# Kernel optimization log

Hardware: AMD Instinct MI355X
Metric: run time of the kernel (lower is better)

Reference implementation:

```python
import jax, jax.numpy as jnp
import numpy as np

NEG_SLOPE = 0.2  # GATConv attention leaky_relu slope (init arg)
POST_SLOPE = 0.2  # leaky_relu after LayerNorm in outer forward
N_LAYERS = 3


def _leaky(x, slope):
    return jnp.where(x >= 0, x, slope * x)


def _layer_norm(x, g, b):
    mu = jnp.mean(x, axis=-1, keepdims=True)
    var = jnp.var(x, axis=-1, keepdims=True)
    return (x - mu) * jax.lax.rsqrt(var + 1e-5) * g + b


def _gat_conv(h, W, al, ar, bias, src, dst, apply_act):
    # DGL GATConv (eval mode, dropout = identity)
    N = h.shape[0]
    H, D = al.shape
    feat = (h @ W).reshape(N, H, D)                      # [N,H,D]
    el = jnp.einsum('nhd,hd->nh', feat, al)              # [N,H]
    er = jnp.einsum('nhd,hd->nh', feat, ar)              # [N,H]
    e = _leaky(el[src] + er[dst], NEG_SLOPE)             # [E,H] edge logits
    # segment (per-destination) softmax, numerically stable
    m = jax.ops.segment_max(e, dst, num_segments=N)      # [N,H]
    ex = jnp.exp(e - m[dst])                             # [E,H]
    s = jax.ops.segment_sum(ex, dst, num_segments=N)     # [N,H]
    alpha = ex / s[dst]                                  # [E,H]
    msg = alpha[:, :, None] * feat[src]                  # [E,H,D]
    rst = jax.ops.segment_sum(msg, dst, num_segments=N)  # [N,H,D]
    rst = rst + bias.reshape(1, H, D)
    if apply_act:
        rst = jax.nn.elu(rst)
    return rst


def setup_inputs() -> dict:
    key = jax.random.key(0)
    ks = jax.random.split(key, 12)
    N, E, IN, D, H, C = 100000, 1600000, 256, 64, 4, 40
    HID = H * D  # 256
    sc = 0.05
    return {
        'x': jax.random.normal(ks[0], (N, IN), jnp.float32),
        'W_h': jax.random.normal(ks[1], (3, IN, HID), jnp.float32) * sc,
        'attn_l_h': jax.random.normal(ks[2], (3, H, D), jnp.float32) * sc,
        'attn_r_h': jax.random.normal(ks[3], (3, H, D), jnp.float32) * sc,
        'bias_h': jnp.zeros((3, HID), jnp.float32),
        'ln_g': jnp.ones((3, HID), jnp.float32),
        'ln_b': jnp.zeros((3, HID), jnp.float32),
        'W_o': jax.random.normal(ks[4], (HID, C), jnp.float32) * sc,
        'attn_l_o': jax.random.normal(ks[5], (1, C), jnp.float32) * sc,
        'attn_r_o': jax.random.normal(ks[6], (1, C), jnp.float32) * sc,
        'bias_o': jnp.zeros((C,), jnp.float32),
        'edge_src': jax.random.randint(ks[7], (E,), 0, N, jnp.int32),
        'edge_dst': jax.random.randint(ks[8], (E,), 0, N, jnp.int32),
    }


def reference(x, W_h, attn_l_h, attn_r_h, bias_h, ln_g, ln_b,
              W_o, attn_l_o, attn_r_o, bias_o, edge_src, edge_dst):
    h = x
    for l in range(N_LAYERS):
        hn = _gat_conv(h, W_h[l], attn_l_h[l], attn_r_h[l], bias_h[l],
                       edge_src, edge_dst, True)
        hn = hn.reshape(hn.shape[0], -1)          # flatten heads -> [N, H*D]
        hn = _layer_norm(hn, ln_g[l], ln_b[l])
        hn = _leaky(hn, POST_SLOPE)
        h = hn + h if h.shape == hn.shape else hn  # residual when shapes match
    logits = _gat_conv(h, W_o, attn_l_o, attn_r_o, bias_o,
                       edge_src, edge_dst, False).sum(axis=1)  # sum over heads
    return logits
```

## Files before the change

### kernel.cpp

```cpp
#include <hip/hip_runtime.h>
#include <math.h>


#define NEG_SLOPE 0.2f

typedef __attribute__((ext_vector_type(8))) short bf16x8;
typedef __attribute__((ext_vector_type(4))) float floatx4;

__device__ __forceinline__ float leaky(float x) { return x >= 0.f ? x : NEG_SLOPE * x; }

__device__ __forceinline__ unsigned short f2bf(float f) {
    unsigned u = __builtin_bit_cast(unsigned, f);
    u += 0x7fffu + ((u >> 16) & 1u);
    return (unsigned short)(u >> 16);
}
__device__ __forceinline__ float bf2f(unsigned short h) {
    unsigned u = ((unsigned)h) << 16;
    return __builtin_bit_cast(float, u);
}

__global__ void zero_i32(int* __restrict__ p, int n) {
    int i = blockIdx.x * blockDim.x + threadIdx.x;
    if (i < n) p[i] = 0;
}

__global__ void hist_kernel(const int* __restrict__ dst, int* __restrict__ counts, int E) {
    int e = blockIdx.x * blockDim.x + threadIdx.x;
    if (e < E) atomicAdd(&counts[dst[e]], 1);
}

__global__ void alloc_kernel(const int* __restrict__ counts, int* __restrict__ start,
                             int* __restrict__ cursor, int* __restrict__ total, int N) {
    int n = blockIdx.x * blockDim.x + threadIdx.x;
    if (n < N) {
        int c = counts[n];
        int s = atomicAdd(total, c);
        start[n] = s;
        cursor[n] = s;
    }
}

__global__ void scatter_kernel(const int* __restrict__ src, const int* __restrict__ dst,
                               int* __restrict__ cursor, int* __restrict__ col, int E) {
    int e = blockIdx.x * blockDim.x + threadIdx.x;
    if (e < E) {
        int p = atomicAdd(&cursor[dst[e]], 1);
        col[p] = src[e];
    }
}

__global__ void convert_bf(const float* __restrict__ src, unsigned short* __restrict__ dst,
                           int n4) {
    int i = blockIdx.x * blockDim.x + threadIdx.x;
    if (i < n4) {
        float4 v = *(const float4*)(src + (size_t)i * 4);
        ushort4 s;
        s.x = f2bf(v.x); s.y = f2bf(v.y); s.z = f2bf(v.z); s.w = f2bf(v.w);
        *(ushort4*)(dst + (size_t)i * 4) = s;
    }
}

__global__ void transpose_w(const float* __restrict__ W, unsigned short* __restrict__ Wt) {
    int idx = blockIdx.x * 256 + threadIdx.x;
    int l = idx >> 16, r = idx & 65535;
    int k = r >> 8, n = r & 255;
    Wt[l * 65536 + n * 256 + k] = f2bf(W[l * 65536 + k * 256 + n]);
}

__global__ void transpose_wo(const float* __restrict__ W, unsigned short* __restrict__ Wt) {
    int idx = blockIdx.x * 256 + threadIdx.x;
    int n = idx >> 8, k = idx & 255;
    Wt[n * 256 + k] = (n < 40) ? f2bf(W[k * 40 + n]) : (unsigned short)0;
}

#define LDSK 40
__global__ __launch_bounds__(256, 2) void gemm_bf16_fused(
    const unsigned short* __restrict__ A, const unsigned short* __restrict__ Wt,
    const float* __restrict__ al, const float* __restrict__ ar,
    unsigned short* __restrict__ Cb, float* __restrict__ el, float* __restrict__ er, int M) {
    __shared__ unsigned short As[128 * LDSK];
    __shared__ unsigned short Bs[128 * LDSK];
    const int tid = threadIdx.x;
    const int bx = blockIdx.x & 1;
    const int by = blockIdx.x >> 1;
    const int row0 = by * 128, col0 = bx * 128;
    const int lane = tid & 63, wid = tid >> 6;
    const int wm = (wid & 1) * 64, wn = (wid >> 1) * 64;

    const int rA = tid >> 2, k8 = (tid & 3) * 8;
    auto loadA = [&](int kb, int rr) -> bf16x8 {
        int gr = row0 + rr;
        bf16x8 v = {};
        if (gr < M) v = *(const bf16x8*)(A + (size_t)gr * 256 + kb + k8);
        return v;
    };
    auto loadB = [&](int kb, int rr) -> bf16x8 {
        return *(const bf16x8*)(Wt + (size_t)(col0 + rr) * 256 + kb + k8);
    };

    floatx4 acc[4][4] = {};
    bf16x8 pa0 = loadA(0, rA), pa1 = loadA(0, rA + 64);
    bf16x8 pb0 = loadB(0, rA), pb1 = loadB(0, rA + 64);

    const int q = lane >> 4, m = lane & 15;
    for (int kb = 0; kb < 256; kb += 32) {
        *(bf16x8*)&As[rA * LDSK + k8] = pa0;
        *(bf16x8*)&As[(rA + 64) * LDSK + k8] = pa1;
        *(bf16x8*)&Bs[rA * LDSK + k8] = pb0;
        *(bf16x8*)&Bs[(rA + 64) * LDSK + k8] = pb1;
        __syncthreads();
        int nkb = kb + 32;
        if (nkb < 256) {
            pa0 = loadA(nkb, rA); pa1 = loadA(nkb, rA + 64);
            pb0 = loadB(nkb, rA); pb1 = loadB(nkb, rA + 64);
        }
        bf16x8 af[4], bfr[4];
#pragma unroll
        for (int i = 0; i < 4; ++i) {
            af[i] = *(const bf16x8*)&As[(wm + i * 16 + m) * LDSK + q * 8];
            bfr[i] = *(const bf16x8*)&Bs[(wn + i * 16 + m) * LDSK + q * 8];
        }
#pragma unroll
        for (int i = 0; i < 4; ++i)
#pragma unroll
            for (int j = 0; j < 4; ++j)
                acc[i][j] = __builtin_amdgcn_mfma_f32_16x16x32_bf16(af[i], bfr[j], acc[i][j], 0, 0, 0);
        __syncthreads();
    }

    const int c = lane & 15;
#pragma unroll
    for (int i = 0; i < 4; ++i)
#pragma unroll
        for (int j = 0; j < 4; ++j)
#pragma unroll
            for (int r = 0; r < 4; ++r) {
                int grow = row0 + wm + i * 16 + q * 4 + r;
                int gcol = col0 + wn + j * 16 + c;
                if (grow < M) Cb[(size_t)grow * 256 + gcol] = f2bf(acc[i][j][r]);
            }

    const int head = bx * 2 + (wn >> 6);
    const float* alh = al + head * 64;
    const float* arh = ar + head * 64;
    float a0 = alh[c], a1 = alh[16 + c], a2 = alh[32 + c], a3 = alh[48 + c];
    float r0 = arh[c], r1 = arh[16 + c], r2 = arh[32 + c], r3 = arh[48 + c];
#pragma unroll
    for (int i = 0; i < 4; ++i)
#pragma unroll
        for (int r = 0; r < 4; ++r) {
            float pel = acc[i][0][r] * a0 + acc[i][1][r] * a1 + acc[i][2][r] * a2 + acc[i][3][r] * a3;
            float per = acc[i][0][r] * r0 + acc[i][1][r] * r1 + acc[i][2][r] * r2 + acc[i][3][r] * r3;
#pragma unroll
            for (int off = 8; off >= 1; off >>= 1) {
                pel += __shfl_xor(pel, off);
                per += __shfl_xor(per, off);
            }
            if (c == 0) {
                int grow = row0 + wm + i * 16 + q * 4 + r;
                if (grow < M) {
                    el[(size_t)grow * 4 + head] = pel;
                    er[(size_t)grow * 4 + head] = per;
                }
            }
        }
}

#define BSTRIDE 264
__global__ __launch_bounds__(256) void gemm_out_mfma(const unsigned short* __restrict__ h,
                                                     const unsigned short* __restrict__ Wt,
                                                     unsigned short* __restrict__ feat_o, int N) {
    __shared__ unsigned short As[128 * LDSK];
    __shared__ unsigned short Bs[48 * BSTRIDE];
    const int tid = threadIdx.x;
    const int row0 = blockIdx.x * 128;
    const int lane = tid & 63, wid = tid >> 6;

#pragma unroll
    for (int i = 0; i < 6; ++i) {
        int f = tid + 256 * i;
        int n = f >> 5, kk = (f & 31) * 8;
        *(bf16x8*)&Bs[n * BSTRIDE + kk] = *(const bf16x8*)(Wt + n * 256 + kk);
    }
    __syncthreads();

    floatx4 acc[2][3] = {};
    for (int kb = 0; kb < 256; kb += 32) {
#pragma unroll
        for (int i = 0; i < 2; ++i) {
            int idx = tid + 256 * i;
            int r = idx >> 2, k8 = (idx & 3) * 8;
            int gr = row0 + r;
            bf16x8 v = {};
            if (gr < N) v = *(const bf16x8*)(h + (size_t)gr * 256 + kb + k8);
            *(bf16x8*)&As[r * LDSK + k8] = v;
        }
        __syncthreads();
        const int q = lane >> 4, m = lane & 15;
        bf16x8 af[2], bfr[3];
#pragma unroll
        for (int i = 0; i < 2; ++i)
            af[i] = *(const bf16x8*)&As[(wid * 32 + i * 16 + m) * LDSK + q * 8];
#pragma unroll
        for (int j = 0; j < 3; ++j)
            bfr[j] = *(const bf16x8*)&Bs[(j * 16 + m) * BSTRIDE + kb + q * 8];
#pragma unroll
        for (int i = 0; i < 2; ++i)
#pragma unroll
            for (int j = 0; j < 3; ++j)
                acc[i][j] = __builtin_amdgcn_mfma_f32_16x16x32_bf16(af[i], bfr[j], acc[i][j], 0, 0, 0);
        __syncthreads();
    }

    const int q = lane >> 4, c = lane & 15;
#pragma unroll
    for (int i = 0; i < 2; ++i)
#pragma unroll
        for (int j = 0; j < 3; ++j)
#pragma unroll
            for (int r = 0; r < 4; ++r) {
                int grow = row0 + wid * 32 + i * 16 + q * 4 + r;
                int gcol = j * 16 + c;
                if (grow < N && gcol < 40) feat_o[(size_t)grow * 40 + gcol] = f2bf(acc[i][j][r]);
            }
}

__global__ __launch_bounds__(256) void scores_out(const unsigned short* __restrict__ feat_o,
                                                  const float* __restrict__ alo,
                                                  const float* __restrict__ aro,
                                                  float* __restrict__ elo,
                                                  float* __restrict__ ero, int N) {
    int node = blockIdx.x * 4 + (threadIdx.x >> 6);
    int lane = threadIdx.x & 63;
    if (node >= N) return;
    float v = 0.f, a = 0.f, r = 0.f;
    if (lane < 40) {
        v = bf2f(feat_o[(size_t)node * 40 + lane]);
        a = alo[lane];
        r = aro[lane];
    }
    float pl = v * a, pr = v * r;
#pragma unroll
    for (int off = 32; off >= 1; off >>= 1) {
        pl += __shfl_xor(pl, off);
        pr += __shfl_xor(pr, off);
    }
    if (lane == 0) {
        elo[node] = pl;
        ero[node] = pr;
    }
}

__global__ __launch_bounds__(256) void aggregate_hidden(
    const unsigned short* __restrict__ feat, const float* __restrict__ el,
    const float* __restrict__ er, const int* __restrict__ start, const int* __restrict__ endp,
    const int* __restrict__ col, const float* __restrict__ bias, const float* __restrict__ lng,
    const float* __restrict__ lnb, const unsigned short* __restrict__ h_in,
    unsigned short* __restrict__ h_out, int N) {
    int node = blockIdx.x * 4 + (threadIdx.x >> 6);
    int lane = threadIdx.x & 63;
    if (node >= N) return;
    int begin = __builtin_amdgcn_readfirstlane(start[node]);
    int end = __builtin_amdgcn_readfirstlane(endp[node]);
    const int head = lane >> 4;
    const float erh = er[(size_t)node * 4 + head];

    const int ch = lane * 4;
    const unsigned short* fbase = feat + ch;
    const size_t hstr = 256;
    float4 acc = {0.f, 0.f, 0.f, 0.f};
    float ssum = 0.f;
    int e = begin;
    for (; e + 7 < end; e += 8) {
        int sA = col[e], sB = col[e + 1], sC = col[e + 2], sD = col[e + 3];
        int sE = col[e + 4], sF = col[e + 5], sG = col[e + 6], sH = col[e + 7];
        float eA = el[(size_t)sA * 4 + head];
        float eB = el[(size_t)sB * 4 + head];
        float eC = el[(size_t)sC * 4 + head];
        float eD = el[(size_t)sD * 4 + head];
        float eE = el[(size_t)sE * 4 + head];
        float eF = el[(size_t)sF * 4 + head];
        float eG = el[(size_t)sG * 4 + head];
        float eH = el[(size_t)sH * 4 + head];
        ushort4 uA = *(const ushort4*)(fbase + sA * hstr);
        ushort4 uB = *(const ushort4*)(fbase + sB * hstr);
        ushort4 uC = *(const ushort4*)(fbase + sC * hstr);
        ushort4 uD = *(const ushort4*)(fbase + sD * hstr);
        ushort4 uE = *(const ushort4*)(fbase + sE * hstr);
        ushort4 uF = *(const ushort4*)(fbase + sF * hstr);
        ushort4 uG = *(const ushort4*)(fbase + sG * hstr);
        ushort4 uH = *(const ushort4*)(fbase + sH * hstr);
        float wA = __expf(leaky(eA + erh));
        float wB = __expf(leaky(eB + erh));
        float wC = __expf(leaky(eC + erh));
        float wD = __expf(leaky(eD + erh));
        float wE = __expf(leaky(eE + erh));
        float wF = __expf(leaky(eF + erh));
        float wG = __expf(leaky(eG + erh));
        float wH = __expf(leaky(eH + erh));
        ssum += wA + wB + wC + wD + wE + wF + wG + wH;
        acc.x = fmaf(wA, bf2f(uA.x), acc.x); acc.y = fmaf(wA, bf2f(uA.y), acc.y);
        acc.z = fmaf(wA, bf2f(uA.z), acc.z); acc.w = fmaf(wA, bf2f(uA.w), acc.w);
        acc.x = fmaf(wB, bf2f(uB.x), acc.x); acc.y = fmaf(wB, bf2f(uB.y), acc.y);
        acc.z = fmaf(wB, bf2f(uB.z), acc.z); acc.w = fmaf(wB, bf2f(uB.w), acc.w);
        acc.x = fmaf(wC, bf2f(uC.x), acc.x); acc.y = fmaf(wC, bf2f(uC.y), acc.y);
        acc.z = fmaf(wC, bf2f(uC.z), acc.z); acc.w = fmaf(wC, bf2f(uC.w), acc.w);
        acc.x = fmaf(wD, bf2f(uD.x), acc.x); acc.y = fmaf(wD, bf2f(uD.y), acc.y);
        acc.z = fmaf(wD, bf2f(uD.z), acc.z); acc.w = fmaf(wD, bf2f(uD.w), acc.w);
        acc.x = fmaf(wE, bf2f(uE.x), acc.x); acc.y = fmaf(wE, bf2f(uE.y), acc.y);
        acc.z = fmaf(wE, bf2f(uE.z), acc.z); acc.w = fmaf(wE, bf2f(uE.w), acc.w);
        acc.x = fmaf(wF, bf2f(uF.x), acc.x); acc.y = fmaf(wF, bf2f(uF.y), acc.y);
        acc.z = fmaf(wF, bf2f(uF.z), acc.z); acc.w = fmaf(wF, bf2f(uF.w), acc.w);
        acc.x = fmaf(wG, bf2f(uG.x), acc.x); acc.y = fmaf(wG, bf2f(uG.y), acc.y);
        acc.z = fmaf(wG, bf2f(uG.z), acc.z); acc.w = fmaf(wG, bf2f(uG.w), acc.w);
        acc.x = fmaf(wH, bf2f(uH.x), acc.x); acc.y = fmaf(wH, bf2f(uH.y), acc.y);
        acc.z = fmaf(wH, bf2f(uH.z), acc.z); acc.w = fmaf(wH, bf2f(uH.w), acc.w);
    }
    for (; e < end; ++e) {
        int sA = col[e];
        float wA = __expf(leaky(el[(size_t)sA * 4 + head] + erh));
        ushort4 uA = *(const ushort4*)(fbase + sA * hstr);
        ssum += wA;
        acc.x = fmaf(wA, bf2f(uA.x), acc.x); acc.y = fmaf(wA, bf2f(uA.y), acc.y);
        acc.z = fmaf(wA, bf2f(uA.z), acc.z); acc.w = fmaf(wA, bf2f(uA.w), acc.w);
    }
    float inv = ssum > 0.f ? 1.f / ssum : 0.f;
    acc.x *= inv; acc.y *= inv; acc.z *= inv; acc.w *= inv;

    float4 bb = *(const float4*)(bias + ch);
    float x0 = acc.x + bb.x, x1 = acc.y + bb.y, x2 = acc.z + bb.z, x3 = acc.w + bb.w;
    x0 = x0 > 0.f ? x0 : expm1f(x0);
    x1 = x1 > 0.f ? x1 : expm1f(x1);
    x2 = x2 > 0.f ? x2 : expm1f(x2);
    x3 = x3 > 0.f ? x3 : expm1f(x3);
    float lsum = x0 + x1 + x2 + x3;
    float lsq = x0 * x0 + x1 * x1 + x2 * x2 + x3 * x3;
#pragma unroll
    for (int off = 32; off >= 1; off >>= 1) {
        lsum += __shfl_xor(lsum, off);
        lsq += __shfl_xor(lsq, off);
    }
    float mu = lsum * (1.f / 256.f);
    float var = lsq * (1.f / 256.f) - mu * mu;
    float rstd = rsqrtf(var + 1e-5f);
    float4 g4 = *(const float4*)(lng + ch);
    float4 b4 = *(const float4*)(lnb + ch);
    ushort4 hi = *(const ushort4*)(h_in + (size_t)node * 256 + ch);
    float y0 = (x0 - mu) * rstd * g4.x + b4.x;
    float y1 = (x1 - mu) * rstd * g4.y + b4.y;
    float y2 = (x2 - mu) * rstd * g4.z + b4.z;
    float y3 = (x3 - mu) * rstd * g4.w + b4.w;
    y0 = (y0 >= 0.f ? y0 : 0.2f * y0) + bf2f(hi.x);
    y1 = (y1 >= 0.f ? y1 : 0.2f * y1) + bf2f(hi.y);
    y2 = (y2 >= 0.f ? y2 : 0.2f * y2) + bf2f(hi.z);
    y3 = (y3 >= 0.f ? y3 : 0.2f * y3) + bf2f(hi.w);
    ushort4 o;
    o.x = f2bf(y0); o.y = f2bf(y1); o.z = f2bf(y2); o.w = f2bf(y3);
    *(ushort4*)(h_out + (size_t)node * 256 + ch) = o;
}

__global__ __launch_bounds__(256) void aggregate_out(const unsigned short* __restrict__ feat_o,
                                                     const float* __restrict__ elo,
                                                     const float* __restrict__ ero,
                                                     const int* __restrict__ start,
                                                     const int* __restrict__ endp,
                                                     const int* __restrict__ col,
                                                     const float* __restrict__ bias_o,
                                                     float* __restrict__ out, int N) {
    int node = blockIdx.x * 4 + (threadIdx.x >> 6);
    int lane = threadIdx.x & 63;
    if (node >= N) return;
    int begin = __builtin_amdgcn_readfirstlane(start[node]);
    int end = __builtin_amdgcn_readfirstlane(endp[node]);
    float ern = ero[node];
    int cc = lane < 40 ? lane : 0;
    float acc = 0.f, ssum = 0.f;
    int e = begin;
    for (; e + 7 < end; e += 8) {
        int sA = col[e], sB = col[e + 1], sC = col[e + 2], sD = col[e + 3];
        int sE = col[e + 4], sF = col[e + 5], sG = col[e + 6], sH = col[e + 7];
        float eA = elo[sA], eB = elo[sB], eC = elo[sC], eD = elo[sD];
        float eE = elo[sE], eF = elo[sF], eG = elo[sG], eH = elo[sH];
        unsigned short fA = feat_o[(size_t)sA * 40 + cc];
        unsigned short fB = feat_o[(size_t)sB * 40 + cc];
        unsigned short fC = feat_o[(size_t)sC * 40 + cc];
        unsigned short fD = feat_o[(size_t)sD * 40 + cc];
        unsigned short fE = feat_o[(size_t)sE * 40 + cc];
        unsigned short fF = feat_o[(size_t)sF * 40 + cc];
        unsigned short fG = feat_o[(size_t)sG * 40 + cc];
        unsigned short fH = feat_o[(size_t)sH * 40 + cc];
        float wA = __expf(leaky(eA + ern));
        float wB = __expf(leaky(eB + ern));
        float wC = __expf(leaky(eC + ern));
        float wD = __expf(leaky(eD + ern));
        float wE = __expf(leaky(eE + ern));
        float wF = __expf(leaky(eF + ern));
        float wG = __expf(leaky(eG + ern));
        float wH = __expf(leaky(eH + ern));
        ssum += wA + wB + wC + wD + wE + wF + wG + wH;
        acc = fmaf(wA, bf2f(fA), acc);
        acc = fmaf(wB, bf2f(fB), acc);
        acc = fmaf(wC, bf2f(fC), acc);
        acc = fmaf(wD, bf2f(fD), acc);
        acc = fmaf(wE, bf2f(fE), acc);
        acc = fmaf(wF, bf2f(fF), acc);
        acc = fmaf(wG, bf2f(fG), acc);
        acc = fmaf(wH, bf2f(fH), acc);
    }
    for (; e < end; ++e) {
        int sA = col[e];
        float wA = __expf(leaky(elo[sA] + ern));
        ssum += wA;
        acc = fmaf(wA, bf2f(feat_o[(size_t)sA * 40 + cc]), acc);
    }
    float inv = ssum > 0.f ? 1.f / ssum : 0.f;
    if (lane < 40) out[(size_t)node * 40 + lane] = acc * inv + bias_o[lane];
}

extern "C" void kernel_launch(void* const* d_in, const int* in_sizes, int n_in,
                              void* d_out, int out_size, void* d_ws, size_t ws_size,
                              hipStream_t stream) {
    const float* x = (const float*)d_in[0];
    const float* W_h = (const float*)d_in[1];
    const float* al_h = (const float*)d_in[2];
    const float* ar_h = (const float*)d_in[3];
    const float* bias_h = (const float*)d_in[4];
    const float* ln_g = (const float*)d_in[5];
    const float* ln_b = (const float*)d_in[6];
    const float* W_o = (const float*)d_in[7];
    const float* al_o = (const float*)d_in[8];
    const float* ar_o = (const float*)d_in[9];
    const float* bias_o = (const float*)d_in[10];
    const int* esrc = (const int*)d_in[11];
    const int* edst = (const int*)d_in[12];
    const int N = in_sizes[0] / 256;
    const int E = in_sizes[11];
    float* out = (float*)d_out;

    char* ws = (char*)d_ws;
    size_t off = 0;
    auto walloc = [&](size_t bytes) -> void* {
        void* p = ws + off;
        off += (bytes + 255) & ~(size_t)255;
        return p;
    };
    unsigned short* x_bf = (unsigned short*)walloc((size_t)N * 256 * 2);
    unsigned short* h_bf = (unsigned short*)walloc((size_t)N * 256 * 2);
    unsigned short* feat_bf = (unsigned short*)walloc((size_t)N * 256 * 2);
    unsigned short* Wt = (unsigned short*)walloc((size_t)3 * 65536 * 2);
    unsigned short* Wt_o = (unsigned short*)walloc((size_t)48 * 256 * 2);
    float* el = (float*)walloc((size_t)N * 4 * 4);
    float* er = (float*)walloc((size_t)N * 4 * 4);
    int* counts = (int*)walloc(((size_t)N + 1) * 4);
    int* start = (int*)walloc((size_t)N * 4);
    int* endp = (int*)walloc((size_t)N * 4);
    int* col = (int*)walloc((size_t)E * 4);
    if (off > ws_size) return;

    const int TB = 256;
    convert_bf<<<(N * 64 + TB - 1) / TB, TB, 0, stream>>>(x, x_bf, N * 64);
    transpose_w<<<3 * 65536 / TB, TB, 0, stream>>>(W_h, Wt);
    transpose_wo<<<48, TB, 0, stream>>>(W_o, Wt_o);
    zero_i32<<<(N + 1 + TB - 1) / TB, TB, 0, stream>>>(counts, N + 1);
    hist_kernel<<<(E + TB - 1) / TB, TB, 0, stream>>>(edst, counts, E);
    alloc_kernel<<<(N + TB - 1) / TB, TB, 0, stream>>>(counts, start, endp, counts + N, N);
    scatter_kernel<<<(E + TB - 1) / TB, TB, 0, stream>>>(esrc, edst, endp, col, E);

    const int nb4 = (N + 3) / 4;
    const int gemm_grid = ((N + 127) / 128) * 2;
    for (int l = 0; l < 3; ++l) {
        const unsigned short* hin = (l == 0) ? x_bf : h_bf;
        gemm_bf16_fused<<<gemm_grid, 256, 0, stream>>>(hin, Wt + (size_t)l * 65536,
                                                       al_h + l * 256, ar_h + l * 256,
                                                       feat_bf, el, er, N);
        aggregate_hidden<<<nb4, 256, 0, stream>>>(feat_bf, el, er, start, endp, col,
                                                  bias_h + l * 256, ln_g + l * 256,
                                                  ln_b + l * 256, hin, h_bf, N);
    }
    unsigned short* feat_o = feat_bf;
    float* elo = el;
    float* ero = er;
    gemm_out_mfma<<<(N + 127) / 128, 256, 0, stream>>>(h_bf, Wt_o, feat_o, N);
    scores_out<<<nb4, 256, 0, stream>>>(feat_o, al_o, ar_o, elo, ero, N);
    aggregate_out<<<nb4, 256, 0, stream>>>(feat_o, elo, ero, start, endp, col, bias_o, out, N);
}
```

Baseline: 1.013 ms.

## Split wave into two half-waves gathering 16B rows; fuse output scores into GEMM

The hidden-layer aggregation now has each half of a wavefront process alternate edges, with each lane loading 8 bf16 channels (16 bytes) instead of 4. The two halves' partial sums are combined by a cross-half shuffle, and the LayerNorm reduction runs within 32 lanes. The aim is more bytes in flight per gather instruction and fewer edge iterations, at the cost of more registers and an extra reduction. Separately, the output-layer attention scores are computed in the GEMM epilogue from the fp32 accumulators, which removes the scores_out kernel launch and the re-read of feat_o.

```diff
diff --git a/kernel.cpp b/kernel.cpp
--- a/kernel.cpp
+++ b/kernel.cpp
@@ -6,6 +6,7 @@
 
 typedef __attribute__((ext_vector_type(8))) short bf16x8;
 typedef __attribute__((ext_vector_type(4))) float floatx4;
+typedef __attribute__((ext_vector_type(8))) unsigned short ushort8v;
 
 __device__ __forceinline__ float leaky(float x) { return x >= 0.f ? x : NEG_SLOPE * x; }
 
@@ -169,7 +170,11 @@
 #define BSTRIDE 264
 __global__ __launch_bounds__(256) void gemm_out_mfma(const unsigned short* __restrict__ h,
                                                      const unsigned short* __restrict__ Wt,
-                                                     unsigned short* __restrict__ feat_o, int N) {
+                                                     const float* __restrict__ alo,
+                                                     const float* __restrict__ aro,
+                                                     unsigned short* __restrict__ feat_o,
+                                                     float* __restrict__ elo,
+                                                     float* __restrict__ ero, int N) {
     __shared__ unsigned short As[128 * LDSK];
     __shared__ unsigned short Bs[48 * BSTRIDE];
     const int tid = threadIdx.x;
@@ -223,32 +228,33 @@
                 int gcol = j * 16 + c;
                 if (grow < N && gcol < 40) feat_o[(size_t)grow * 40 + gcol] = f2bf(acc[i][j][r]);
             }
-}
-
-__global__ __launch_bounds__(256) void scores_out(const unsigned short* __restrict__ feat_o,
-                                                  const float* __restrict__ alo,
-                                                  const float* __restrict__ aro,
-                                                  float* __restrict__ elo,
-                                                  float* __restrict__ ero, int N) {
-    int node = blockIdx.x * 4 + (threadIdx.x >> 6);
-    int lane = threadIdx.x & 63;
-    if (node >= N) return;
-    float v = 0.f, a = 0.f, r = 0.f;
-    if (lane < 40) {
-        v = bf2f(feat_o[(size_t)node * 40 + lane]);
-        a = alo[lane];
-        r = aro[lane];
-    }
-    float pl = v * a, pr = v * r;
-#pragma unroll
-    for (int off = 32; off >= 1; off >>= 1) {
-        pl += __shfl_xor(pl, off);
-        pr += __shfl_xor(pr, off);
-    }
-    if (lane == 0) {
-        elo[node] = pl;
-        ero[node] = pr;
-    }
+
+    float aj[3], rj[3];
+#pragma unroll
+    for (int j = 0; j < 3; ++j) {
+        int gcol = j * 16 + c;
+        aj[j] = gcol < 40 ? alo[gcol] : 0.f;
+        rj[j] = gcol < 40 ? aro[gcol] : 0.f;
+    }
+#pragma unroll
+    for (int i = 0; i < 2; ++i)
+#pragma unroll
+        for (int r = 0; r < 4; ++r) {
+            float pl = acc[i][0][r] * aj[0] + acc[i][1][r] * aj[1] + acc[i][2][r] * aj[2];
+            float pr = acc[i][0][r] * rj[0] + acc[i][1][r] * rj[1] + acc[i][2][r] * rj[2];
+#pragma unroll
+            for (int off = 8; off >= 1; off >>= 1) {
+                pl += __shfl_xor(pl, off);
+                pr += __shfl_xor(pr, off);
+            }
+            if (c == 0) {
+                int grow = row0 + wid * 32 + i * 16 + q * 4 + r;
+                if (grow < N) {
+                    elo[grow] = pl;
+                    ero[grow] = pr;
+                }
+            }
+        }
 }
 
 __global__ __launch_bounds__(256) void aggregate_hidden(
@@ -262,101 +268,106 @@
     if (node >= N) return;
     int begin = __builtin_amdgcn_readfirstlane(start[node]);
     int end = __builtin_amdgcn_readfirstlane(endp[node]);
-    const int head = lane >> 4;
+    const int hl = lane & 31;
+    const int half = lane >> 5;
+    const int head = hl >> 3;
     const float erh = er[(size_t)node * 4 + head];
-
-    const int ch = lane * 4;
+    const int ch = hl * 8;
     const unsigned short* fbase = feat + ch;
-    const size_t hstr = 256;
-    float4 acc = {0.f, 0.f, 0.f, 0.f};
+
+    float acc[8] = {};
     float ssum = 0.f;
     int e = begin;
     for (; e + 7 < end; e += 8) {
-        int sA = col[e], sB = col[e + 1], sC = col[e + 2], sD = col[e + 3];
-        int sE = col[e + 4], sF = col[e + 5], sG = col[e + 6], sH = col[e + 7];
+        int c0 = col[e], c1 = col[e + 1], c2 = col[e + 2], c3 = col[e + 3];
+        int c4 = col[e + 4], c5 = col[e + 5], c6 = col[e + 6], c7 = col[e + 7];
+        int sA = half ? c1 : c0;
+        int sB = half ? c3 : c2;
+        int sC = half ? c5 : c4;
+        int sD = half ? c7 : c6;
         float eA = el[(size_t)sA * 4 + head];
         float eB = el[(size_t)sB * 4 + head];
         float eC = el[(size_t)sC * 4 + head];
         float eD = el[(size_t)sD * 4 + head];
-        float eE = el[(size_t)sE * 4 + head];
-        float eF = el[(size_t)sF * 4 + head];
-        float eG = el[(size_t)sG * 4 + head];
-        float eH = el[(size_t)sH * 4 + head];
-        ushort4 uA = *(const ushort4*)(fbase + sA * hstr);
-        ushort4 uB = *(const ushort4*)(fbase + sB * hstr);
-        ushort4 uC = *(const ushort4*)(fbase + sC * hstr);
-        ushort4 uD = *(const ushort4*)(fbase + sD * hstr);
-        ushort4 uE = *(const ushort4*)(fbase + sE * hstr);
-        ushort4 uF = *(const ushort4*)(fbase + sF * hstr);
-        ushort4 uG = *(const ushort4*)(fbase + sG * hstr);
-        ushort4 uH = *(const ushort4*)(fbase + sH * hstr);
+        ushort8v uA = *(const ushort8v*)(fbase + (size_t)sA * 256);
+        ushort8v uB = *(const ushort8v*)(fbase + (size_t)sB * 256);
+        ushort8v uC = *(const ushort8v*)(fbase + (size_t)sC * 256);
+        ushort8v uD = *(const ushort8v*)(fbase + (size_t)sD * 256);
         float wA = __expf(leaky(eA + erh));
         float wB = __expf(leaky(eB + erh));
         float wC = __expf(leaky(eC + erh));
         float wD = __expf(leaky(eD + erh));
-        float wE = __expf(leaky(eE + erh));
-        float wF = __expf(leaky(eF + erh));
-        float wG = __expf(leaky(eG + erh));
-        float wH = __expf(leaky(eH + erh));
-        ssum += wA + wB + wC + wD + wE + wF + wG + wH;
-        acc.x = fmaf(wA, bf2f(uA.x), acc.x); acc.y = fmaf(wA, bf2f(uA.y), acc.y);
-        acc.z = fmaf(wA, bf2f(uA.z), acc.z); acc.w = fmaf(wA, bf2f(uA.w), acc.w);
-        acc.x = fmaf(wB, bf2f(uB.x), acc.x); acc.y = fmaf(wB, bf2f(uB.y), acc.y);
-        acc.z = fmaf(wB, bf2f(uB.z), acc.z); acc.w = fmaf(wB, bf2f(uB.w), acc.w);
-        acc.x = fmaf(wC, bf2f(uC.x), acc.x); acc.y = fmaf(wC, bf2f(uC.y), acc.y);
-        acc.z = fmaf(wC, bf2f(uC.z), acc.z); acc.w = fmaf(wC, bf2f(uC.w), acc.w);
-        acc.x = fmaf(wD, bf2f(uD.x), acc.x); acc.y = fmaf(wD, bf2f(uD.y), acc.y);
-        acc.z = fmaf(wD, bf2f(uD.z), acc.z); acc.w = fmaf(wD, bf2f(uD.w), acc.w);
-        acc.x = fmaf(wE, bf2f(uE.x), acc.x); acc.y = fmaf(wE, bf2f(uE.y), acc.y);
-        acc.z = fmaf(wE, bf2f(uE.z), acc.z); acc.w = fmaf(wE, bf2f(uE.w), acc.w);
-        acc.x = fmaf(wF, bf2f(uF.x), acc.x); acc.y = fmaf(wF, bf2f(uF.y), acc.y);
-        acc.z = fmaf(wF, bf2f(uF.z), acc.z); acc.w = fmaf(wF, bf2f(uF.w), acc.w);
-        acc.x = fmaf(wG, bf2f(uG.x), acc.x); acc.y = fmaf(wG, bf2f(uG.y), acc.y);
-        acc.z = fmaf(wG, bf2f(uG.z), acc.z); acc.w = fmaf(wG, bf2f(uG.w), acc.w);
-        acc.x = fmaf(wH, bf2f(uH.x), acc.x); acc.y = fmaf(wH, bf2f(uH.y), acc.y);
-        acc.z = fmaf(wH, bf2f(uH.z), acc.z); acc.w = fmaf(wH, bf2f(uH.w), acc.w);
-    }
-    for (; e < end; ++e) {
-        int sA = col[e];
-        float wA = __expf(leaky(el[(size_t)sA * 4 + head] + erh));
-        ushort4 uA = *(const ushort4*)(fbase + sA * hstr);
-        ssum += wA;
-        acc.x = fmaf(wA, bf2f(uA.x), acc.x); acc.y = fmaf(wA, bf2f(uA.y), acc.y);
-        acc.z = fmaf(wA, bf2f(uA.z), acc.z); acc.w = fmaf(wA, bf2f(uA.w), acc.w);
-    }
+        ssum += wA + wB + wC + wD;
+#pragma unroll
+        for (int i = 0; i < 8; ++i) {
+            acc[i] = fmaf(wA, bf2f(uA[i]), acc[i]);
+            acc[i] = fmaf(wB, bf2f(uB[i]), acc[i]);
+            acc[i] = fmaf(wC, bf2f(uC[i]), acc[i]);
+            acc[i] = fmaf(wD, bf2f(uD[i]), acc[i]);
+        }
+    }
+    for (; e + 1 < end; e += 2) {
+        int c0 = col[e], c1 = col[e + 1];
+        int s = half ? c1 : c0;
+        float ee = el[(size_t)s * 4 + head];
+        ushort8v u = *(const ushort8v*)(fbase + (size_t)s * 256);
+        float w = __expf(leaky(ee + erh));
+        ssum += w;
+#pragma unroll
+        for (int i = 0; i < 8; ++i) acc[i] = fmaf(w, bf2f(u[i]), acc[i]);
+    }
+    if (e < end) {
+        int s = col[e];
+        float ee = el[(size_t)s * 4 + head];
+        ushort8v u = *(const ushort8v*)(fbase + (size_t)s * 256);
+        float w = half ? 0.f : __expf(leaky(ee + erh));
+        ssum += w;
+#pragma unroll
+        for (int i = 0; i < 8; ++i) acc[i] = fmaf(w, bf2f(u[i]), acc[i]);
+    }
+
+    ssum += __shfl_xor(ssum, 32);
+#pragma unroll
+    for (int i = 0; i < 8; ++i) acc[i] += __shfl_xor(acc[i], 32);
     float inv = ssum > 0.f ? 1.f / ssum : 0.f;
-    acc.x *= inv; acc.y *= inv; acc.z *= inv; acc.w *= inv;
-
-    float4 bb = *(const float4*)(bias + ch);
-    float x0 = acc.x + bb.x, x1 = acc.y + bb.y, x2 = acc.z + bb.z, x3 = acc.w + bb.w;
-    x0 = x0 > 0.f ? x0 : expm1f(x0);
-    x1 = x1 > 0.f ? x1 : expm1f(x1);
-    x2 = x2 > 0.f ? x2 : expm1f(x2);
-    x3 = x3 > 0.f ? x3 : expm1f(x3);
-    float lsum = x0 + x1 + x2 + x3;
-    float lsq = x0 * x0 + x1 * x1 + x2 * x2 + x3 * x3;
-#pragma unroll
-    for (int off = 32; off >= 1; off >>= 1) {
+
+    float4 b0 = *(const float4*)(bias + ch);
+    float4 b1 = *(const float4*)(bias + ch + 4);
+    float bb[8] = {b0.x, b0.y, b0.z, b0.w, b1.x, b1.y, b1.z, b1.w};
+    float x[8];
+    float lsum = 0.f, lsq = 0.f;
+#pragma unroll
+    for (int i = 0; i < 8; ++i) {
+        float v = acc[i] * inv + bb[i];
+        v = v > 0.f ? v : expm1f(v);
+        x[i] = v;
+        lsum += v;
+        lsq += v * v;
+    }
+#pragma unroll
+    for (int off = 16; off >= 1; off >>= 1) {
         lsum += __shfl_xor(lsum, off);
         lsq += __shfl_xor(lsq, off);
     }
     float mu = lsum * (1.f / 256.f);
     float var = lsq * (1.f / 256.f) - mu * mu;
     float rstd = rsqrtf(var + 1e-5f);
-    float4 g4 = *(const float4*)(lng + ch);
-    float4 b4 = *(const float4*)(lnb + ch);
-    ushort4 hi = *(const ushort4*)(h_in + (size_t)node * 256 + ch);
-    float y0 = (x0 - mu) * rstd * g4.x + b4.x;
-    float y1 = (x1 - mu) * rstd * g4.y + b4.y;
-    float y2 = (x2 - mu) * rstd * g4.z + b4.z;
-    float y3 = (x3 - mu) * rstd * g4.w + b4.w;
-    y0 = (y0 >= 0.f ? y0 : 0.2f * y0) + bf2f(hi.x);
-    y1 = (y1 >= 0.f ? y1 : 0.2f * y1) + bf2f(hi.y);
-    y2 = (y2 >= 0.f ? y2 : 0.2f * y2) + bf2f(hi.z);
-    y3 = (y3 >= 0.f ? y3 : 0.2f * y3) + bf2f(hi.w);
-    ushort4 o;
-    o.x = f2bf(y0); o.y = f2bf(y1); o.z = f2bf(y2); o.w = f2bf(y3);
-    *(ushort4*)(h_out + (size_t)node * 256 + ch) = o;
+    if (half) return;
+    float4 g0 = *(const float4*)(lng + ch);
+    float4 g1 = *(const float4*)(lng + ch + 4);
+    float4 p0 = *(const float4*)(lnb + ch);
+    float4 p1 = *(const float4*)(lnb + ch + 4);
+    float gg[8] = {g0.x, g0.y, g0.z, g0.w, g1.x, g1.y, g1.z, g1.w};
+    float pp[8] = {p0.x, p0.y, p0.z, p0.w, p1.x, p1.y, p1.z, p1.w};
+    ushort8v hi8 = *(const ushort8v*)(h_in + (size_t)node * 256 + ch);
+    ushort8v o;
+#pragma unroll
+    for (int i = 0; i < 8; ++i) {
+        float y = (x[i] - mu) * rstd * gg[i] + pp[i];
+        y = (y >= 0.f ? y : 0.2f * y) + bf2f(hi8[i]);
+        o[i] = f2bf(y);
+    }
+    *(ushort8v*)(h_out + (size_t)node * 256 + ch) = o;
 }
 
 __global__ __launch_bounds__(256) void aggregate_out(const unsigned short* __restrict__ feat_o,
@@ -480,7 +491,6 @@
     unsigned short* feat_o = feat_bf;
     float* elo = el;
     float* ero = er;
-    gemm_out_mfma<<<(N + 127) / 128, 256, 0, stream>>>(h_bf, Wt_o, feat_o, N);
-    scores_out<<<nb4, 256, 0, stream>>>(feat_o, al_o, ar_o, elo, ero, N);
+    gemm_out_mfma<<<(N + 127) / 128, 256, 0, stream>>>(h_bf, Wt_o, al_o, ar_o, feat_o, elo, ero, N);
     aggregate_out<<<nb4, 256, 0, stream>>>(feat_o, elo, ero, start, endp, col, bias_o, out, N);
 }
```

Result: no change. 1.001 ms (-1.2%).

## Double-buffer hidden GEMM with direct global-to-LDS loads and fuse output scores

Applied to the files above, without the earlier changes.

The hidden-layer GEMM now uses 512-thread blocks, each covering all 256 output columns for 128 rows. Tiles are staged straight into double-buffered LDS with global_load_lds, so the A tile is read once instead of twice, one barrier per k-step is dropped, and register round-trips go away. The output GEMM now computes the el/er attention scores in its epilogue, which removes the separate scores_out kernel and its reread of feat_o. The trade-offs are more LDS per block, unpadded 32-wide LDS rows that may cause bank conflicts, and reliance on the async load being complete at the barrier.

```diff
diff --git a/kernel.cpp b/kernel.cpp
--- a/kernel.cpp
+++ b/kernel.cpp
@@ -17,6 +17,12 @@
 __device__ __forceinline__ float bf2f(unsigned short h) {
     unsigned u = ((unsigned)h) << 16;
     return __builtin_bit_cast(float, u);
+}
+
+typedef const __attribute__((address_space(1))) unsigned int* as1_u32p;
+typedef __attribute__((address_space(3))) unsigned int* as3_u32p;
+__device__ __forceinline__ void gl_lds16(const void* g, void* l) {
+    __builtin_amdgcn_global_load_lds((as1_u32p)g, (as3_u32p)l, 16, 0, 0);
 }
 
 __global__ void zero_i32(int* __restrict__ p, int n) {
@@ -73,52 +79,43 @@
     Wt[n * 256 + k] = (n < 40) ? f2bf(W[k * 40 + n]) : (unsigned short)0;
 }
 
-#define LDSK 40
-__global__ __launch_bounds__(256, 2) void gemm_bf16_fused(
+__global__ __launch_bounds__(512, 4) void gemm_bf16_fused(
     const unsigned short* __restrict__ A, const unsigned short* __restrict__ Wt,
     const float* __restrict__ al, const float* __restrict__ ar,
     unsigned short* __restrict__ Cb, float* __restrict__ el, float* __restrict__ er, int M) {
-    __shared__ unsigned short As[128 * LDSK];
-    __shared__ unsigned short Bs[128 * LDSK];
+    __shared__ unsigned short As[2][128 * 32];
+    __shared__ unsigned short Bs[2][256 * 32];
     const int tid = threadIdx.x;
-    const int bx = blockIdx.x & 1;
-    const int by = blockIdx.x >> 1;
-    const int row0 = by * 128, col0 = bx * 128;
+    const int row0 = blockIdx.x * 128;
     const int lane = tid & 63, wid = tid >> 6;
-    const int wm = (wid & 1) * 64, wn = (wid >> 1) * 64;
-
-    const int rA = tid >> 2, k8 = (tid & 3) * 8;
-    auto loadA = [&](int kb, int rr) -> bf16x8 {
-        int gr = row0 + rr;
-        bf16x8 v = {};
-        if (gr < M) v = *(const bf16x8*)(A + (size_t)gr * 256 + kb + k8);
-        return v;
+    const int wm = (wid >> 2) * 64;
+    const int wn = (wid & 3) * 64;
+
+    const int arow = wid * 16 + (lane >> 2);
+    const int brow0 = wid * 32 + (lane >> 2);
+    const int kx = (lane & 3) * 8;
+    const int agr = (row0 + arow < M) ? (row0 + arow) : (M - 1);
+
+    auto stage = [&](int buf, int kb) {
+        gl_lds16(A + (size_t)agr * 256 + kb + kx, &As[buf][arow * 32 + kx]);
+        gl_lds16(Wt + (size_t)brow0 * 256 + kb + kx, &Bs[buf][brow0 * 32 + kx]);
+        gl_lds16(Wt + (size_t)(brow0 + 16) * 256 + kb + kx, &Bs[buf][(brow0 + 16) * 32 + kx]);
     };
-    auto loadB = [&](int kb, int rr) -> bf16x8 {
-        return *(const bf16x8*)(Wt + (size_t)(col0 + rr) * 256 + kb + k8);
-    };
 
     floatx4 acc[4][4] = {};
-    bf16x8 pa0 = loadA(0, rA), pa1 = loadA(0, rA + 64);
-    bf16x8 pb0 = loadB(0, rA), pb1 = loadB(0, rA + 64);
-
     const int q = lane >> 4, m = lane & 15;
+
+    stage(0, 0);
+    __syncthreads();
+    int cur = 0;
     for (int kb = 0; kb < 256; kb += 32) {
-        *(bf16x8*)&As[rA * LDSK + k8] = pa0;
-        *(bf16x8*)&As[(rA + 64) * LDSK + k8] = pa1;
-        *(bf16x8*)&Bs[rA * LDSK + k8] = pb0;
-        *(bf16x8*)&Bs[(rA + 64) * LDSK + k8] = pb1;
-        __syncthreads();
         int nkb = kb + 32;
-        if (nkb < 256) {
-            pa0 = loadA(nkb, rA); pa1 = loadA(nkb, rA + 64);
-            pb0 = loadB(nkb, rA); pb1 = loadB(nkb, rA + 64);
-        }
+        if (nkb < 256) stage(cur ^ 1, nkb);
         bf16x8 af[4], bfr[4];
 #pragma unroll
         for (int i = 0; i < 4; ++i) {
-            af[i] = *(const bf16x8*)&As[(wm + i * 16 + m) * LDSK + q * 8];
-            bfr[i] = *(const bf16x8*)&Bs[(wn + i * 16 + m) * LDSK + q * 8];
+            af[i] = *(const bf16x8*)&As[cur][(wm + i * 16 + m) * 32 + q * 8];
+            bfr[i] = *(const bf16x8*)&Bs[cur][(wn + i * 16 + m) * 32 + q * 8];
         }
 #pragma unroll
         for (int i = 0; i < 4; ++i)
@@ -126,6 +123,7 @@
             for (int j = 0; j < 4; ++j)
                 acc[i][j] = __builtin_amdgcn_mfma_f32_16x16x32_bf16(af[i], bfr[j], acc[i][j], 0, 0, 0);
         __syncthreads();
+        cur ^= 1;
     }
 
     const int c = lane & 15;
@@ -136,11 +134,11 @@
 #pragma unroll
             for (int r = 0; r < 4; ++r) {
                 int grow = row0 + wm + i * 16 + q * 4 + r;
-                int gcol = col0 + wn + j * 16 + c;
+                int gcol = wn + j * 16 + c;
                 if (grow < M) Cb[(size_t)grow * 256 + gcol] = f2bf(acc[i][j][r]);
             }
 
-    const int head = bx * 2 + (wn >> 6);
+    const int head = wid & 3;
     const float* alh = al + head * 64;
     const float* arh = ar + head * 64;
     float a0 = alh[c], a1 = alh[16 + c], a2 = alh[32 + c], a3 = alh[48 + c];
@@ -166,10 +164,15 @@
         }
 }
 
+#define LDSK 40
 #define BSTRIDE 264
 __global__ __launch_bounds__(256) void gemm_out_mfma(const unsigned short* __restrict__ h,
                                                      const unsigned short* __restrict__ Wt,
-                                                     unsigned short* __restrict__ feat_o, int N) {
+                                                     const float* __restrict__ alo,
+                                                     const float* __restrict__ aro,
+                                                     unsigned short* __restrict__ feat_o,
+                                                     float* __restrict__ elo,
+                                                     float* __restrict__ ero, int N) {
     __shared__ unsigned short As[128 * LDSK];
     __shared__ unsigned short Bs[48 * BSTRIDE];
     const int tid = threadIdx.x;
@@ -223,32 +226,33 @@
                 int gcol = j * 16 + c;
                 if (grow < N && gcol < 40) feat_o[(size_t)grow * 40 + gcol] = f2bf(acc[i][j][r]);
             }
-}
-
-__global__ __launch_bounds__(256) void scores_out(const unsigned short* __restrict__ feat_o,
-                                                  const float* __restrict__ alo,
-                                                  const float* __restrict__ aro,
-                                                  float* __restrict__ elo,
-                                                  float* __restrict__ ero, int N) {
-    int node = blockIdx.x * 4 + (threadIdx.x >> 6);
-    int lane = threadIdx.x & 63;
-    if (node >= N) return;
-    float v = 0.f, a = 0.f, r = 0.f;
-    if (lane < 40) {
-        v = bf2f(feat_o[(size_t)node * 40 + lane]);
-        a = alo[lane];
-        r = aro[lane];
-    }
-    float pl = v * a, pr = v * r;
-#pragma unroll
-    for (int off = 32; off >= 1; off >>= 1) {
-        pl += __shfl_xor(pl, off);
-        pr += __shfl_xor(pr, off);
-    }
-    if (lane == 0) {
-        elo[node] = pl;
-        ero[node] = pr;
-    }
+
+    float aj[3], rj[3];
+#pragma unroll
+    for (int j = 0; j < 3; ++j) {
+        int gcol = j * 16 + c;
+        aj[j] = gcol < 40 ? alo[gcol] : 0.f;
+        rj[j] = gcol < 40 ? aro[gcol] : 0.f;
+    }
+#pragma unroll
+    for (int i = 0; i < 2; ++i)
+#pragma unroll
+        for (int r = 0; r < 4; ++r) {
+            float pl = acc[i][0][r] * aj[0] + acc[i][1][r] * aj[1] + acc[i][2][r] * aj[2];
+            float pr = acc[i][0][r] * rj[0] + acc[i][1][r] * rj[1] + acc[i][2][r] * rj[2];
+#pragma unroll
+            for (int off = 8; off >= 1; off >>= 1) {
+                pl += __shfl_xor(pl, off);
+                pr += __shfl_xor(pr, off);
+            }
+            if (c == 0) {
+                int grow = row0 + wid * 32 + i * 16 + q * 4 + r;
+                if (grow < N) {
+                    elo[grow] = pl;
+                    ero[grow] = pr;
+                }
+            }
+        }
 }
 
 __global__ __launch_bounds__(256) void aggregate_hidden(
@@ -467,10 +471,10 @@
     scatter_kernel<<<(E + TB - 1) / TB, TB, 0, stream>>>(esrc, edst, endp, col, E);
 
     const int nb4 = (N + 3) / 4;
-    const int gemm_grid = ((N + 127) / 128) * 2;
+    const int gemm_grid = (N + 127) / 128;
     for (int l = 0; l < 3; ++l) {
         const unsigned short* hin = (l == 0) ? x_bf : h_bf;
-        gemm_bf16_fused<<<gemm_grid, 256, 0, stream>>>(hin, Wt + (size_t)l * 65536,
+        gemm_bf16_fused<<<gemm_grid, 512, 0, stream>>>(hin, Wt + (size_t)l * 65536,
                                                        al_h + l * 256, ar_h + l * 256,
                                                        feat_bf, el, er, N);
         aggregate_hidden<<<nb4, 256, 0, stream>>>(feat_bf, el, er, start, endp, col,
@@ -480,7 +484,6 @@
     unsigned short* feat_o = feat_bf;
     float* elo = el;
     float* ero = er;
-    gemm_out_mfma<<<(N + 127) / 128, 256, 0, stream>>>(h_bf, Wt_o, feat_o, N);
-    scores_out<<<nb4, 256, 0, stream>>>(feat_o, al_o, ar_o, elo, ero, N);
+    gemm_out_mfma<<<(N + 127) / 128, 256, 0, stream>>>(h_bf, Wt_o, al_o, ar_o, feat_o, elo, ero, N);
     aggregate_out<<<nb4, 256, 0, stream>>>(feat_o, elo, ero, start, endp, col, bias_o, out, N);
 }
```

Measured after the change: 986.9 us. 2.5% less time.
